# Performance work log

Measured on AMD Instinct MI355X. Metric: run time of the kernel, lower is better.

Reference implementation:

```python
import jax, jax.numpy as jnp
import numpy as np
import math

HEADS = 8
HIDDEN = 512
HEAD_DIM = HIDDEN // HEADS
BATCH = 16
N = 512
ALPHA = 1.0 / math.sqrt(HEAD_DIM)


def setup_inputs() -> dict:
    key = jax.random.key(0)
    ks = jax.random.split(key, 6)
    stdv_qkv = 1.0 / math.sqrt(HEAD_DIM)
    stdv_o = 1.0 / math.sqrt(HIDDEN)
    return {
        "x": jax.random.normal(ks[0], (BATCH, N, HIDDEN), dtype=jnp.float32),
        "edge": jax.random.normal(ks[1], (HEADS, BATCH, N, N), dtype=jnp.float32),
        "Wq": jax.random.uniform(ks[2], (HEADS, HIDDEN, HEAD_DIM), jnp.float32, -stdv_qkv, stdv_qkv),
        "Wk": jax.random.uniform(ks[3], (HEADS, HIDDEN, HEAD_DIM), jnp.float32, -stdv_qkv, stdv_qkv),
        "Wv": jax.random.uniform(ks[4], (HEADS, HIDDEN, HEAD_DIM), jnp.float32, -stdv_qkv, stdv_qkv),
        "Wo": jax.random.uniform(ks[5], (HIDDEN, HIDDEN), jnp.float32, -stdv_o, stdv_o),
    }


def reference(x, edge, Wq, Wk, Wv, Wo):
    # per-head projections: x [b,n,h] x W [g,h,d] -> [g,b,n,d]
    Q = jnp.einsum("bnh,ghd->gbnd", x, Wq)
    K = jnp.einsum("bnh,ghd->gbnd", x, Wk)
    V = jnp.einsum("bnh,ghd->gbnd", x, Wv)
    # edge-biased attention scores [g,b,n,n]
    S = edge + ALPHA * jnp.einsum("gbnd,gbmd->gbnm", Q, K)
    S = jax.nn.softmax(S, axis=-1)
    # attend and merge heads: [g,b,n,d] -> [b,n,g*d]
    o = jnp.einsum("gbnm,gbmd->bngd", S, V)
    o = o.reshape(o.shape[0], o.shape[1], -1)
    return o @ Wo
```

## Files before the change

### kernel.cpp

```cpp
#include <hip/hip_runtime.h>

typedef __bf16 bf16;
typedef __bf16 bf16x4 __attribute__((ext_vector_type(4)));
typedef __bf16 bf16x8 __attribute__((ext_vector_type(8)));
typedef float f32x4 __attribute__((ext_vector_type(4)));

#define ALPHA_ 0.125f


__device__ __forceinline__ void gload16(const void* g, void* l) {
  __builtin_amdgcn_global_load_lds((__attribute__((address_space(1))) void*)(g),
                                   (__attribute__((address_space(3))) void*)(l),
                                   16, 0, 0);
}

__global__ void cast_x_kernel(const float* __restrict__ x, bf16* __restrict__ xb) {
  int i = blockIdx.x * 256 + threadIdx.x;
  float4 v = ((const float4*)x)[i];
  bf16x4 o = {(bf16)v.x, (bf16)v.y, (bf16)v.z, (bf16)v.w};
  ((bf16x4*)xb)[i] = o;
}

__global__ void prep_w_kernel(const float* __restrict__ Wq, const float* __restrict__ Wk,
                              const float* __restrict__ Wv, bf16* __restrict__ wcat) {
  int i = blockIdx.x * 256 + threadIdx.x;
  int h = i & 511, j = i >> 9;
  int qkv = j >> 9, g = (j >> 6) & 7, d = j & 63;
  const float* W = (qkv == 0) ? Wq : ((qkv == 1) ? Wk : Wv);
  wcat[i] = (bf16)W[((g << 9) + h) * 64 + d];
}

__global__ void prep_wo_kernel(const float* __restrict__ Wo, bf16* __restrict__ wot) {
  int i = blockIdx.x * 256 + threadIdx.x;
  int k = i & 511, n = i >> 9;
  wot[i] = (bf16)Wo[(k << 9) + n];
}

template <int MODE>
__global__ __launch_bounds__(256, 2) void gemm_bt_kernel(
    const bf16* __restrict__ A, const bf16* __restrict__ Bt, int Kdim, int Ndim,
    float* __restrict__ Cf, bf16* __restrict__ Qo, bf16* __restrict__ Ko,
    bf16* __restrict__ Vto) {
  __shared__ bf16 lA[128 * 32];
  __shared__ bf16 lB[128 * 32];
  const int t = threadIdx.x;
  const int w = t >> 6;
  const int lane = t & 63;
  const int lhi = lane >> 4, llo = lane & 15;
  const int m0 = blockIdx.y * 128, n0 = blockIdx.x * 128;
  const int wr = (w >> 1) * 64, wc = (w & 1) * 64;

  f32x4 acc[4][4] = {};
  const int nkt = Kdim >> 5;
  for (int kt = 0; kt < nkt; ++kt) {
#pragma unroll
    for (int c = 0; c < 2; ++c) {
      int u = c * 256 + t;
      const bf16* ga = A + (size_t)(m0 + (u >> 2)) * Kdim + kt * 32 + (u & 3) * 8;
      gload16(ga, &lA[c * 2048 + w * 512]);
      const bf16* gb = Bt + (size_t)(n0 + (u >> 2)) * Kdim + kt * 32 + (u & 3) * 8;
      gload16(gb, &lB[c * 2048 + w * 512]);
    }
    __syncthreads();
    bf16x8 af[4], bfr[4];
#pragma unroll
    for (int i = 0; i < 4; ++i) {
      af[i] = *(const bf16x8*)&lA[(wr + i * 16 + llo) * 32 + lhi * 8];
      bfr[i] = *(const bf16x8*)&lB[(wc + i * 16 + llo) * 32 + lhi * 8];
    }
#pragma unroll
    for (int i = 0; i < 4; ++i)
#pragma unroll
      for (int j = 0; j < 4; ++j)
        acc[i][j] = __builtin_amdgcn_mfma_f32_16x16x32_bf16(af[i], bfr[j], acc[i][j], 0, 0, 0);
    __syncthreads();
  }

#pragma unroll
  for (int i = 0; i < 4; ++i) {
    int row = m0 + wr + i * 16 + lhi * 4;
#pragma unroll
    for (int j = 0; j < 4; ++j) {
      int col = n0 + wc + j * 16 + llo;
#pragma unroll
      for (int r = 0; r < 4; ++r) {
        float v = acc[i][j][r];
        int rr = row + r;
        if (MODE == 0) {
          int qkv = col >> 9, g = (col >> 6) & 7, d = col & 63;
          bf16 bv = (bf16)v;
          if (qkv == 0)
            Qo[((size_t)g * 8192 + rr) * 64 + d] = bv;
          else if (qkv == 1)
            Ko[((size_t)g * 8192 + rr) * 64 + d] = bv;
          else {
            int b = rr >> 9, n = rr & 511;
            Vto[(((size_t)g * 16 + b) * 64 + d) * 512 + n] = bv;
          }
        } else {
          Cf[(size_t)rr * Ndim + col] = v;
        }
      }
    }
  }
}

__global__ __launch_bounds__(256, 4) void attn_kernel(
    const bf16* __restrict__ Qa, const bf16* __restrict__ Ka,
    const bf16* __restrict__ Vta, const float* __restrict__ edge,
    bf16* __restrict__ Oatt) {
  __shared__ bf16 lK[2][64 * 64];
  __shared__ bf16 lV[2][64 * 64];
  const int t = threadIdx.x, w = t >> 6, lane = t & 63;
  const int lhi = lane >> 4, llo = lane & 15;
  const int qt = blockIdx.x, b = blockIdx.y, g = blockIdx.z;
  const int q0 = qt * 64 + w * 16;
  const bf16* Qg = Qa + ((size_t)g * 8192 + b * 512) * 64;
  const bf16* Kg = Ka + ((size_t)g * 8192 + b * 512) * 64;
  const bf16* Vg = Vta + ((size_t)g * 16 + b) * (64 * 512);
  const float* eg = edge + ((size_t)g * 16 + b) * (512 * 512);

  bf16x8 qf[2];
#pragma unroll
  for (int ks = 0; ks < 2; ++ks)
    qf[ks] = *(const bf16x8*)(Qg + (size_t)(q0 + llo) * 64 + ks * 32 + lhi * 8);

  f32x4 oacc[4] = {};
  float mrow = -3e38f, lrow = 0.f;

  const int r0 = t >> 3;
  const int r1 = r0 + 32;
  const int cs = (((t & 7) ^ (r0 & 7)) << 3);

  f32x4 eb[2][4];

  gload16(Kg + (size_t)r0 * 64 + cs, &lK[0][w * 512]);
  gload16(Kg + (size_t)r1 * 64 + cs, &lK[0][2048 + w * 512]);
  gload16(Vg + (size_t)r0 * 512 + cs, &lV[0][w * 512]);
  gload16(Vg + (size_t)r1 * 512 + cs, &lV[0][2048 + w * 512]);
#pragma unroll
  for (int ni = 0; ni < 4; ++ni)
    eb[0][ni] = *(const f32x4*)(eg + (size_t)(q0 + llo) * 512 + ni * 16 + lhi * 4);
  __builtin_amdgcn_sched_barrier(0);

#pragma unroll
  for (int it = 0; it < 8; ++it) {
    const int cur = it & 1, nxt = cur ^ 1;
    const int kv0 = it * 64;

    if (it < 7) {
      const int kvn = kv0 + 64;
      gload16(Kg + (size_t)(kvn + r0) * 64 + cs, &lK[nxt][w * 512]);
      gload16(Kg + (size_t)(kvn + r1) * 64 + cs, &lK[nxt][2048 + w * 512]);
      gload16(Vg + (size_t)r0 * 512 + kvn + cs, &lV[nxt][w * 512]);
      gload16(Vg + (size_t)r1 * 512 + kvn + cs, &lV[nxt][2048 + w * 512]);
#pragma unroll
      for (int ni = 0; ni < 4; ++ni)
        eb[nxt][ni] = *(const f32x4*)(eg + (size_t)(q0 + llo) * 512 + kvn + ni * 16 + lhi * 4);
    }
    __builtin_amdgcn_sched_barrier(0);
    if (it < 7)
      asm volatile("s_waitcnt vmcnt(8)" ::: "memory");
    else
      asm volatile("s_waitcnt vmcnt(0)" ::: "memory");
    __builtin_amdgcn_sched_barrier(0);
    __builtin_amdgcn_s_barrier();
    __builtin_amdgcn_sched_barrier(0);

    f32x4 sc[4] = {};
    __builtin_amdgcn_s_setprio(1);
#pragma unroll
    for (int ks = 0; ks < 2; ++ks) {
      bf16x8 kf[4];
#pragma unroll
      for (int ni = 0; ni < 4; ++ni) {
        int row = ni * 16 + llo;
        kf[ni] = *(const bf16x8*)&lK[cur][(row * 64 + ks * 32 + lhi * 8) ^ ((row & 7) << 3)];
      }
#pragma unroll
      for (int ni = 0; ni < 4; ++ni)
        sc[ni] = __builtin_amdgcn_mfma_f32_16x16x32_bf16(kf[ni], qf[ks], sc[ni], 0, 0, 0);
    }
    __builtin_amdgcn_s_setprio(0);

    float mx = -3e38f;
#pragma unroll
    for (int ni = 0; ni < 4; ++ni)
#pragma unroll
      for (int r = 0; r < 4; ++r) {
        float sv = fmaf(ALPHA_, sc[ni][r], eb[cur][ni][r]);
        sc[ni][r] = sv;
        mx = fmaxf(mx, sv);
      }
    mx = fmaxf(mx, __shfl_xor(mx, 16));
    mx = fmaxf(mx, __shfl_xor(mx, 32));
    float mnew = fmaxf(mrow, mx);
    float s = __expf(mrow - mnew);
    mrow = mnew;
    float rsum = 0.f;
#pragma unroll
    for (int ni = 0; ni < 4; ++ni)
#pragma unroll
      for (int r = 0; r < 4; ++r) {
        float p = __expf(sc[ni][r] - mnew);
        sc[ni][r] = p;
        rsum += p;
      }
    rsum += __shfl_xor(rsum, 16);
    rsum += __shfl_xor(rsum, 32);
    lrow = lrow * s + rsum;

#pragma unroll
    for (int r = 0; r < 4; ++r) {
      float sq = __shfl(s, (lane & 48) | (lhi * 4 + r));
#pragma unroll
      for (int nc = 0; nc < 4; ++nc) oacc[nc][r] *= sq;
    }

    __builtin_amdgcn_s_setprio(1);
#pragma unroll
    for (int ks2 = 0; ks2 < 2; ++ks2) {
      const int n0 = ks2 * 2, n1 = n0 + 1;
      unsigned xa, xb, ya, yb;
      asm("v_cvt_pk_bf16_f32 %0, %1, %2" : "=v"(xa) : "v"(sc[n0][0]), "v"(sc[n0][1]));
      asm("v_cvt_pk_bf16_f32 %0, %1, %2" : "=v"(xb) : "v"(sc[n0][2]), "v"(sc[n0][3]));
      asm("v_cvt_pk_bf16_f32 %0, %1, %2" : "=v"(ya) : "v"(sc[n1][0]), "v"(sc[n1][1]));
      asm("v_cvt_pk_bf16_f32 %0, %1, %2" : "=v"(yb) : "v"(sc[n1][2]), "v"(sc[n1][3]));
      asm("v_permlane32_swap_b32 %0, %1" : "+v"(xa), "+v"(ya));
      asm("v_permlane16_swap_b32 %0, %1" : "+v"(xa), "+v"(ya));
      asm("v_permlane32_swap_b32 %0, %1" : "+v"(xb), "+v"(yb));
      asm("v_permlane16_swap_b32 %0, %1" : "+v"(xb), "+v"(yb));
      union { unsigned wd[4]; bf16x8 v; } fu;
      fu.wd[0] = xa; fu.wd[1] = xb; fu.wd[2] = ya; fu.wd[3] = yb;
      bf16x8 pf = fu.v;

      bf16x8 vf[4];
#pragma unroll
      for (int nc = 0; nc < 4; ++nc) {
        int row = nc * 16 + llo;
        vf[nc] = *(const bf16x8*)&lV[cur][(row * 64 + ks2 * 32 + lhi * 8) ^ ((row & 7) << 3)];
      }
#pragma unroll
      for (int nc = 0; nc < 4; ++nc)
        oacc[nc] = __builtin_amdgcn_mfma_f32_16x16x32_bf16(pf, vf[nc], oacc[nc], 0, 0, 0);
    }
    __builtin_amdgcn_s_setprio(0);

    if (it < 7) {
      __builtin_amdgcn_sched_barrier(0);
      __builtin_amdgcn_s_barrier();
      __builtin_amdgcn_sched_barrier(0);
    }
  }

  float rcpl = 1.0f / lrow;
#pragma unroll
  for (int r = 0; r < 4; ++r) {
    float lr = __shfl(rcpl, (lane & 48) | (lhi * 4 + r));
    int qrow = q0 + lhi * 4 + r;
#pragma unroll
    for (int nc = 0; nc < 4; ++nc) {
      float ov = oacc[nc][r] * lr;
      Oatt[((size_t)b * 512 + qrow) * 512 + g * 64 + nc * 16 + llo] = (bf16)ov;
    }
  }
}

extern "C" void kernel_launch(void* const* d_in, const int* in_sizes, int n_in,
                              void* d_out, int out_size, void* d_ws, size_t ws_size,
                              hipStream_t stream) {
  (void)in_sizes; (void)n_in; (void)out_size; (void)ws_size;
  const float* x = (const float*)d_in[0];
  const float* edge = (const float*)d_in[1];
  const float* Wq = (const float*)d_in[2];
  const float* Wk = (const float*)d_in[3];
  const float* Wv = (const float*)d_in[4];
  const float* Wo = (const float*)d_in[5];
  float* out = (float*)d_out;

  char* ws = (char*)d_ws;
  bf16* xb   = (bf16*)(ws + 0);
  bf16* wcat = (bf16*)(ws + 8388608);
  bf16* wot  = (bf16*)(ws + 9961472);
  bf16* Qa   = (bf16*)(ws + 10485760);
  bf16* Ka   = (bf16*)(ws + 18874368);
  bf16* Vta  = (bf16*)(ws + 27262976);
  bf16* Oatt = (bf16*)(ws + 35651584);

  cast_x_kernel<<<4096, 256, 0, stream>>>(x, xb);
  prep_w_kernel<<<3072, 256, 0, stream>>>(Wq, Wk, Wv, wcat);
  prep_wo_kernel<<<1024, 256, 0, stream>>>(Wo, wot);

  gemm_bt_kernel<0><<<dim3(12, 64), 256, 0, stream>>>(xb, wcat, 512, 1536,
                                                      nullptr, Qa, Ka, Vta);
  attn_kernel<<<dim3(8, 16, 8), 256, 0, stream>>>(Qa, Ka, Vta, edge, Oatt);
  gemm_bt_kernel<1><<<dim3(4, 64), 256, 0, stream>>>(Oatt, wot, 512, 512,
                                                     out, nullptr, nullptr, nullptr);
}
```

Before: 106.2 us.

## Stage K/V tiles through registers instead of direct global-to-LDS loads

Replaces the async global_load_lds prefetch of K and V tiles with register-staged loads: the next tile is loaded into VGPRs during the current iteration and written to the alternate LDS buffer at the top of the next one. This removes the trailing per-iteration barrier, leaving one barrier per iteration. The edge-bias prefetch moves from a double-buffered register set to a single set reloaded after the softmax stage. It costs extra VGPRs and ds_write instructions, and the compiler's waitcnt placement now decides how much load latency is actually hidden.

```diff
diff --git a/kernel.cpp b/kernel.cpp
--- a/kernel.cpp
+++ b/kernel.cpp
@@ -111,10 +111,10 @@
     bf16* __restrict__ Oatt) {
   __shared__ bf16 lK[2][64 * 64];
   __shared__ bf16 lV[2][64 * 64];
-  const int t = threadIdx.x, w = t >> 6, lane = t & 63;
+  const int t = threadIdx.x, lane = t & 63;
   const int lhi = lane >> 4, llo = lane & 15;
   const int qt = blockIdx.x, b = blockIdx.y, g = blockIdx.z;
-  const int q0 = qt * 64 + w * 16;
+  const int q0 = qt * 64 + (t >> 6) * 16;
   const bf16* Qg = Qa + ((size_t)g * 8192 + b * 512) * 64;
   const bf16* Kg = Ka + ((size_t)g * 8192 + b * 512) * 64;
   const bf16* Vg = Vta + ((size_t)g * 16 + b) * (64 * 512);
@@ -130,39 +130,34 @@
 
   const int r0 = t >> 3;
   const int r1 = r0 + 32;
-  const int cs = (((t & 7) ^ (r0 & 7)) << 3);
-
-  f32x4 eb[2][4];
-
-  gload16(Kg + (size_t)r0 * 64 + cs, &lK[0][w * 512]);
-  gload16(Kg + (size_t)r1 * 64 + cs, &lK[0][2048 + w * 512]);
-  gload16(Vg + (size_t)r0 * 512 + cs, &lV[0][w * 512]);
-  gload16(Vg + (size_t)r1 * 512 + cs, &lV[0][2048 + w * 512]);
+  const int c8 = (t & 7) * 8;
+  const int lw0 = (r0 * 64 + c8) ^ ((r0 & 7) << 3);
+  const int lw1 = (r1 * 64 + c8) ^ ((r0 & 7) << 3);
+
+  bf16x8 k0s = *(const bf16x8*)(Kg + (size_t)r0 * 64 + c8);
+  bf16x8 k1s = *(const bf16x8*)(Kg + (size_t)r1 * 64 + c8);
+  bf16x8 v0s = *(const bf16x8*)(Vg + (size_t)r0 * 512 + c8);
+  bf16x8 v1s = *(const bf16x8*)(Vg + (size_t)r1 * 512 + c8);
+  f32x4 ef[4];
 #pragma unroll
   for (int ni = 0; ni < 4; ++ni)
-    eb[0][ni] = *(const f32x4*)(eg + (size_t)(q0 + llo) * 512 + ni * 16 + lhi * 4);
-  __builtin_amdgcn_sched_barrier(0);
+    ef[ni] = *(const f32x4*)(eg + (size_t)(q0 + llo) * 512 + ni * 16 + lhi * 4);
 
 #pragma unroll
   for (int it = 0; it < 8; ++it) {
-    const int cur = it & 1, nxt = cur ^ 1;
-    const int kv0 = it * 64;
-
+    const int cur = it & 1;
+    *(bf16x8*)&lK[cur][lw0] = k0s;
+    *(bf16x8*)&lK[cur][lw1] = k1s;
+    *(bf16x8*)&lV[cur][lw0] = v0s;
+    *(bf16x8*)&lV[cur][lw1] = v1s;
     if (it < 7) {
-      const int kvn = kv0 + 64;
-      gload16(Kg + (size_t)(kvn + r0) * 64 + cs, &lK[nxt][w * 512]);
-      gload16(Kg + (size_t)(kvn + r1) * 64 + cs, &lK[nxt][2048 + w * 512]);
-      gload16(Vg + (size_t)r0 * 512 + kvn + cs, &lV[nxt][w * 512]);
-      gload16(Vg + (size_t)r1 * 512 + kvn + cs, &lV[nxt][2048 + w * 512]);
-#pragma unroll
-      for (int ni = 0; ni < 4; ++ni)
-        eb[nxt][ni] = *(const f32x4*)(eg + (size_t)(q0 + llo) * 512 + kvn + ni * 16 + lhi * 4);
-    }
-    __builtin_amdgcn_sched_barrier(0);
-    if (it < 7)
-      asm volatile("s_waitcnt vmcnt(8)" ::: "memory");
-    else
-      asm volatile("s_waitcnt vmcnt(0)" ::: "memory");
+      const int kvn = (it + 1) * 64;
+      k0s = *(const bf16x8*)(Kg + (size_t)(kvn + r0) * 64 + c8);
+      k1s = *(const bf16x8*)(Kg + (size_t)(kvn + r1) * 64 + c8);
+      v0s = *(const bf16x8*)(Vg + (size_t)r0 * 512 + kvn + c8);
+      v1s = *(const bf16x8*)(Vg + (size_t)r1 * 512 + kvn + c8);
+    }
+    asm volatile("s_waitcnt lgkmcnt(0)" ::: "memory");
     __builtin_amdgcn_sched_barrier(0);
     __builtin_amdgcn_s_barrier();
     __builtin_amdgcn_sched_barrier(0);
@@ -188,7 +183,7 @@
     for (int ni = 0; ni < 4; ++ni)
 #pragma unroll
       for (int r = 0; r < 4; ++r) {
-        float sv = fmaf(ALPHA_, sc[ni][r], eb[cur][ni][r]);
+        float sv = fmaf(ALPHA_, sc[ni][r], ef[ni][r]);
         sc[ni][r] = sv;
         mx = fmaxf(mx, sv);
       }
@@ -209,6 +204,13 @@
     rsum += __shfl_xor(rsum, 16);
     rsum += __shfl_xor(rsum, 32);
     lrow = lrow * s + rsum;
+
+    if (it < 7) {
+      const int kvn = (it + 1) * 64;
+#pragma unroll
+      for (int ni = 0; ni < 4; ++ni)
+        ef[ni] = *(const f32x4*)(eg + (size_t)(q0 + llo) * 512 + kvn + ni * 16 + lhi * 4);
+    }
 
 #pragma unroll
     for (int r = 0; r < 4; ++r) {
@@ -245,12 +247,6 @@
         oacc[nc] = __builtin_amdgcn_mfma_f32_16x16x32_bf16(pf, vf[nc], oacc[nc], 0, 0, 0);
     }
     __builtin_amdgcn_s_setprio(0);
-
-    if (it < 7) {
-      __builtin_amdgcn_sched_barrier(0);
-      __builtin_amdgcn_s_barrier();
-      __builtin_amdgcn_sched_barrier(0);
-    }
   }
 
   float rcpl = 1.0f / lrow;
```

After: 111.2 us. 1.05x slower.
